# Performance work log

Hardware: AMD Instinct MI355X
Metric: run time of the kernel (lower is better)

Reference implementation:

```python
import jax, jax.numpy as jnp
import numpy as np

D_MODEL = 1024
N_HEADS = 16
HEAD_DIM = D_MODEL // N_HEADS
NEG_INF = -1e9


def setup_inputs() -> dict:
    key = jax.random.key(0)
    ks = jax.random.split(key, 6)
    B, T, C = 4, 2048, D_MODEL
    x = jax.random.normal(ks[0], (B, T, C), dtype=jnp.float32)
    # causal mask, broadcastable over batch and heads
    mask = jnp.tril(jnp.ones((T, T), dtype=jnp.int32))[None, None]
    scale = 1.0 / np.sqrt(C)
    W_qkv = jax.random.normal(ks[1], (3 * C, C), dtype=jnp.float32) * scale
    b_qkv = jnp.zeros((3 * C,), dtype=jnp.float32)
    W_out = jax.random.normal(ks[2], (C, C), dtype=jnp.float32) * scale
    b_out = jnp.zeros((C,), dtype=jnp.float32)
    return {"x": x, "mask": mask, "W_qkv": W_qkv, "b_qkv": b_qkv,
            "W_out": W_out, "b_out": b_out}


def reference(x, mask, W_qkv, b_qkv, W_out, b_out):
    B, T, C = x.shape
    H, D = N_HEADS, HEAD_DIM
    qkv = x @ W_qkv.T + b_qkv                      # [B, T, 3C]
    q, k, v = jnp.split(qkv, 3, axis=-1)
    # [B, T, C] -> [B, H, T, D]
    q = q.reshape(B, T, H, D).transpose(0, 2, 1, 3)
    k = k.reshape(B, T, H, D).transpose(0, 2, 1, 3)
    v = v.reshape(B, T, H, D).transpose(0, 2, 1, 3)
    scores = jnp.einsum("bhqd,bhkd->bhqk", q, k) / np.sqrt(D)
    scores = jnp.where(mask == 0, NEG_INF, scores)
    att = jax.nn.softmax(scores, axis=-1)          # dropout p=0 (eval)
    out = jnp.einsum("bhqk,bhkd->bhqd", att, v)    # [B, H, T, D]
    out = out.transpose(0, 2, 1, 3).reshape(B, T, C)
    return out @ W_out.T + b_out
```

## Files before the change

### kernel.cpp

```cpp
#include <hip/hip_runtime.h>
#include <hip/hip_bf16.h>

typedef unsigned short u16;
typedef unsigned int u32;
using short8 = __attribute__((ext_vector_type(8))) short;
using f32x4  = __attribute__((ext_vector_type(4))) float;
using f32x16 = __attribute__((ext_vector_type(16))) float;
using uint2v = __attribute__((ext_vector_type(2))) u32;

#define T_SEQ 2048
#define C_DIM 1024
#define NH 16
#define HD 64

#if __has_builtin(__builtin_amdgcn_exp2f)
#define EXP2(x) __builtin_amdgcn_exp2f(x)
#else
#define EXP2(x) exp2f(x)
#endif

__device__ __forceinline__ u16 f2bf(float f) {
    unsigned int u = __float_as_uint(f);
    unsigned int r = (u + 0x7fffu + ((u >> 16) & 1u)) >> 16;
    return (u16)r;
}
__device__ __forceinline__ u32 cvtpk(float lo, float hi) {
    u32 r;
    asm("v_cvt_pk_bf16_f32 %0, %1, %2" : "=v"(r) : "v"(lo), "v"(hi));
    return r;
}
__device__ __forceinline__ short8 mk8(u32 a, u32 b, u32 c, u32 d) {
    union { u32 u[4]; short8 s; } t;
    t.u[0] = a; t.u[1] = b; t.u[2] = c; t.u[3] = d;
    return t.s;
}
__device__ __forceinline__ void gl_lds16(const u16* g, u16* l) {
    __builtin_amdgcn_global_load_lds(
        (const __attribute__((address_space(1))) unsigned int*)g,
        (__attribute__((address_space(3))) unsigned int*)l, 16, 0, 0);
}
template <int N> __device__ __forceinline__ void s_vmcnt();
template <> __device__ __forceinline__ void s_vmcnt<0>() {
    asm volatile("s_waitcnt vmcnt(0)" ::: "memory");
}
template <> __device__ __forceinline__ void s_vmcnt<4>() {
    asm volatile("s_waitcnt vmcnt(4)" ::: "memory");
}
__device__ __forceinline__ void BAR() {
    asm volatile("" ::: "memory");
    __builtin_amdgcn_s_barrier();
    asm volatile("" ::: "memory");
}

__global__ __launch_bounds__(256) void cvt_f32_bf16(const float* __restrict__ in,
                                                    u16* __restrict__ out, int n8) {
    int i = blockIdx.x * blockDim.x + threadIdx.x;
    if (i >= n8) return;
    const float4* p = (const float4*)in + (size_t)i * 2;
    float4 a = p[0], b = p[1];
    short8 o;
    o[0] = (short)f2bf(a.x); o[1] = (short)f2bf(a.y);
    o[2] = (short)f2bf(a.z); o[3] = (short)f2bf(a.w);
    o[4] = (short)f2bf(b.x); o[5] = (short)f2bf(b.y);
    o[6] = (short)f2bf(b.z); o[7] = (short)f2bf(b.w);
    *(short8*)(out + (size_t)i * 8) = o;
}

template <int EPI>
__global__ __launch_bounds__(256) void gemm_bt(const u16* __restrict__ A,
                                               const u16* __restrict__ Bt,
                                               const float* __restrict__ bias,
                                               u16* __restrict__ qb, u16* __restrict__ kb,
                                               u16* __restrict__ vb, float* __restrict__ Cf,
                                               int M, int N, int K) {
    __shared__ __align__(16) u16 Al[2][128][32];
    __shared__ __align__(16) u16 Bl[2][128][32];
    const int tid = threadIdx.x;
    const int lane = tid & 63, wid = tid >> 6;
    const int li = lane & 15, g = lane >> 4;
    const int wr = (wid >> 1) * 64, wc = (wid & 1) * 64;
    const size_t m0 = (size_t)blockIdx.y * 128, n0 = (size_t)blockIdx.x * 128;

    const int srow = lane >> 2;
    const int sch = (lane & 3) ^ ((srow >> 1) & 3);
    const u16* aA = A + (m0 + wid * 32 + srow) * (size_t)K + sch * 8;
    const u16* aB = Bt + (n0 + wid * 32 + srow) * (size_t)K + sch * 8;

    f32x4 acc[4][4] = {};
    const int nt = K / 32;

    auto STAGE = [&](int buf, int k0) {
        gl_lds16(aA + k0, &Al[buf][wid * 32][0]);
        gl_lds16(aA + 16 * (size_t)K + k0, &Al[buf][wid * 32 + 16][0]);
        gl_lds16(aB + k0, &Bl[buf][wid * 32][0]);
        gl_lds16(aB + 16 * (size_t)K + k0, &Bl[buf][wid * 32 + 16][0]);
    };

    STAGE(0, 0);
#pragma unroll 2
    for (int t = 0; t < nt; ++t) {
        if (t + 1 < nt) { STAGE((t + 1) & 1, (t + 1) * 32); s_vmcnt<4>(); }
        else            { s_vmcnt<0>(); }
        BAR();
        short8 af[4], bf[4];
#pragma unroll
        for (int i = 0; i < 4; i++) {
            int row = wr + i * 16 + li;
            af[i] = *(const short8*)&Al[t & 1][row][(g ^ ((row >> 1) & 3)) * 8];
        }
#pragma unroll
        for (int i = 0; i < 4; i++) {
            int row = wc + i * 16 + li;
            bf[i] = *(const short8*)&Bl[t & 1][row][(g ^ ((row >> 1) & 3)) * 8];
        }
        __builtin_amdgcn_s_setprio(1);
#pragma unroll
        for (int mi = 0; mi < 4; mi++)
#pragma unroll
            for (int ni = 0; ni < 4; ni++)
                acc[mi][ni] = __builtin_amdgcn_mfma_f32_16x16x32_bf16(af[mi], bf[ni],
                                                                      acc[mi][ni], 0, 0, 0);
        __builtin_amdgcn_s_setprio(0);
        BAR();
    }

#pragma unroll
    for (int mi = 0; mi < 4; mi++)
#pragma unroll
        for (int ni = 0; ni < 4; ni++)
#pragma unroll
            for (int r = 0; r < 4; r++) {
                size_t row = m0 + wr + mi * 16 + g * 4 + r;
                size_t col = n0 + wc + ni * 16 + li;
                float val = acc[mi][ni][r] + bias[col];
                if (EPI == 0) {
                    int which = (int)(col >> 10);
                    int rem = (int)(col & 1023);
                    int h = rem >> 6, d = rem & 63;
                    size_t b = row >> 11, t = row & 2047;
                    if (which == 0) val *= 0.18033688f;
                    u16* dst = (which == 0) ? qb : (which == 1) ? kb : vb;
                    dst[(((b * NH) + h) * T_SEQ + t) * HD + d] = f2bf(val);
                } else {
                    Cf[row * (size_t)N + col] = val;
                }
            }
}

__global__ __launch_bounds__(256) void vtrans(const u16* __restrict__ V,
                                              u16* __restrict__ Vt) {
    __shared__ u16 L[128][72];
    const int tid = threadIdx.x;
    const int bh = blockIdx.y;
    const int t0 = blockIdx.x * 128;
    {
        int r = tid >> 1, cb = (tid & 1) * 32;
        const u16* src = V + ((size_t)bh * T_SEQ + t0 + r) * HD + cb;
#pragma unroll
        for (int j = 0; j < 4; j++)
            *(short8*)&L[r][cb + j * 8] = *(const short8*)(src + j * 8);
    }
    __syncthreads();
    {
        int d = tid >> 2, ts = (tid & 3) * 32;
        u16* dst = Vt + ((size_t)bh * HD + d) * T_SEQ + t0 + ts;
#pragma unroll
        for (int c = 0; c < 4; c++) {
            short8 o;
#pragma unroll
            for (int j = 0; j < 8; j++) o[j] = (short)L[ts + c * 8 + j][d];
            *(short8*)(dst + c * 8) = o;
        }
    }
}

__global__ __launch_bounds__(256) void attn_fwd2(const u16* __restrict__ Q,
                                                 const u16* __restrict__ K,
                                                 const u16* __restrict__ Vt,
                                                 u16* __restrict__ O) {
    __shared__ __align__(16) u16 KL[2][64 * 64];
    __shared__ __align__(16) u16 VL[2][64 * 64];
    const int tid = threadIdx.x;
    const int lane = tid & 63, wid = tid >> 6;
    const int l31 = lane & 31, hi = lane >> 5;

    const int wg = blockIdx.x;
    const int xcd = wg & 7, idx = wg >> 3;
    const int bh = (xcd << 3) | (idx >> 3);
    const int pair = idx & 7;
    const size_t bhT = (size_t)bh * T_SEQ;
    const int srow8 = lane >> 3, sch = lane & 7;
    const int b = bh >> 4, h = bh & 15;
    const int x7 = l31 & 7;

    for (int seg = 0; seg < 2; ++seg) {
        const int qt = seg ? pair : (15 - pair);
        const int q0 = qt * 128;
        const int qw0 = q0 + wid * 32;
        const int nkt = 2 * qt + 2;

        short8 qf[4];
        {
            const u16* qp = Q + (bhT + qw0 + l31) * HD + hi * 8;
#pragma unroll
            for (int s = 0; s < 4; s++) qf[s] = *(const short8*)(qp + s * 16);
        }

        f32x16 o0 = {}, o1 = {};
        float l_run = 0.f;

#pragma unroll
        for (int i = 0; i < 2; i++) {
            int row = wid * 16 + i * 8 + srow8;
            int ch = sch ^ (row & 7);
            gl_lds16(K + (bhT + row) * HD + ch * 8, &KL[0][(wid * 16 + i * 8) * 64]);
            gl_lds16(Vt + ((size_t)bh * HD + row) * T_SEQ + ch * 8,
                     &VL[0][(wid * 16 + i * 8) * 64]);
        }

        for (int kt = 0; kt < nkt; kt++) {
            __syncthreads();
            if (kt + 1 < nkt) {
                const int kv0n = (kt + 1) * 64;
                const int nb = (kt + 1) & 1;
#pragma unroll
                for (int i = 0; i < 2; i++) {
                    int row = wid * 16 + i * 8 + srow8;
                    int ch = sch ^ (row & 7);
                    gl_lds16(K + (bhT + kv0n + row) * HD + ch * 8,
                             &KL[nb][(wid * 16 + i * 8) * 64]);
                    gl_lds16(Vt + ((size_t)bh * HD + row) * T_SEQ + kv0n + ch * 8,
                             &VL[nb][(wid * 16 + i * 8) * 64]);
                }
            }
            const int kv0 = kt * 64;
            if (kv0 > qw0) continue;
            const u16* KLb = KL[kt & 1];
            const u16* VLb = VL[kt & 1];

            f32x16 s0 = {}, s1 = {};
            __builtin_amdgcn_s_setprio(1);
#pragma unroll
            for (int sl = 0; sl < 4; sl++) {
                int ch = ((sl * 2 + hi) ^ x7) * 8;
                short8 ka = *(const short8*)&KLb[l31 * 64 + ch];
                s0 = __builtin_amdgcn_mfma_f32_32x32x16_bf16(ka, qf[sl], s0, 0, 0, 0);
                short8 kb2 = *(const short8*)&KLb[(32 + l31) * 64 + ch];
                s1 = __builtin_amdgcn_mfma_f32_32x32x16_bf16(kb2, qf[sl], s1, 0, 0, 0);
            }
            __builtin_amdgcn_s_setprio(0);

            const int qg = qw0 + l31;
            if (kv0 + 63 > qw0) {
#pragma unroll
                for (int r = 0; r < 16; r++) {
                    int kvr = kv0 + (r & 3) + 8 * (r >> 2) + 4 * hi;
                    if (kvr > qg) s0[r] = -1e30f;
                    if (kvr + 32 > qg) s1[r] = -1e30f;
                }
            }

            float ls = 0.f;
#pragma unroll
            for (int r = 0; r < 16; r++) {
                float p0 = EXP2(s0[r]);
                float p1 = EXP2(s1[r]);
                s0[r] = p0; s1[r] = p1;
                ls += p0 + p1;
            }
            ls += __shfl_xor(ls, 32);
            l_run += ls;

            {
                u32 c0 = cvtpk(s0[0], s0[1]),   c1 = cvtpk(s0[2], s0[3]),
                    c2 = cvtpk(s0[4], s0[5]),   c3 = cvtpk(s0[6], s0[7]),
                    c4 = cvtpk(s0[8], s0[9]),   c5 = cvtpk(s0[10], s0[11]),
                    c6 = cvtpk(s0[12], s0[13]), c7 = cvtpk(s0[14], s0[15]);
                uint2v wA = __builtin_amdgcn_permlane32_swap(c0, c2, false, false);
                uint2v wB = __builtin_amdgcn_permlane32_swap(c1, c3, false, false);
                uint2v wC = __builtin_amdgcn_permlane32_swap(c4, c6, false, false);
                uint2v wD = __builtin_amdgcn_permlane32_swap(c5, c7, false, false);
                short8 paA = mk8(wA[0], wB[0], wA[1], wB[1]);
                short8 paB = mk8(wC[0], wD[0], wC[1], wD[1]);
                __builtin_amdgcn_s_setprio(1);
#pragma unroll
                for (int sl = 0; sl < 2; sl++) {
                    short8 pa = (sl == 0) ? paA : paB;
                    int ch = ((sl * 2 + hi) ^ x7) * 8;
                    short8 va = *(const short8*)&VLb[l31 * 64 + ch];
                    o0 = __builtin_amdgcn_mfma_f32_32x32x16_bf16(pa, va, o0, 0, 0, 0);
                    short8 vb2 = *(const short8*)&VLb[(32 + l31) * 64 + ch];
                    o1 = __builtin_amdgcn_mfma_f32_32x32x16_bf16(pa, vb2, o1, 0, 0, 0);
                }
                __builtin_amdgcn_s_setprio(0);
            }
            {
                u32 c0 = cvtpk(s1[0], s1[1]),   c1 = cvtpk(s1[2], s1[3]),
                    c2 = cvtpk(s1[4], s1[5]),   c3 = cvtpk(s1[6], s1[7]),
                    c4 = cvtpk(s1[8], s1[9]),   c5 = cvtpk(s1[10], s1[11]),
                    c6 = cvtpk(s1[12], s1[13]), c7 = cvtpk(s1[14], s1[15]);
                uint2v wA = __builtin_amdgcn_permlane32_swap(c0, c2, false, false);
                uint2v wB = __builtin_amdgcn_permlane32_swap(c1, c3, false, false);
                uint2v wC = __builtin_amdgcn_permlane32_swap(c4, c6, false, false);
                uint2v wD = __builtin_amdgcn_permlane32_swap(c5, c7, false, false);
                short8 paC = mk8(wA[0], wB[0], wA[1], wB[1]);
                short8 paD = mk8(wC[0], wD[0], wC[1], wD[1]);
                __builtin_amdgcn_s_setprio(1);
#pragma unroll
                for (int sl = 2; sl < 4; sl++) {
                    short8 pa = (sl == 2) ? paC : paD;
                    int ch = ((sl * 2 + hi) ^ x7) * 8;
                    short8 va = *(const short8*)&VLb[l31 * 64 + ch];
                    o0 = __builtin_amdgcn_mfma_f32_32x32x16_bf16(pa, va, o0, 0, 0, 0);
                    short8 vb2 = *(const short8*)&VLb[(32 + l31) * 64 + ch];
                    o1 = __builtin_amdgcn_mfma_f32_32x32x16_bf16(pa, vb2, o1, 0, 0, 0);
                }
                __builtin_amdgcn_s_setprio(0);
            }
        }

        const float inv = 1.0f / l_run;
#pragma unroll
        for (int r = 0; r < 16; r++) {
            int qr = (r & 3) + 8 * (r >> 2) + 4 * hi;
            float invr = __shfl(inv, qr);
            int t = q0 + wid * 32 + qr;
            size_t rowoff = ((size_t)b * T_SEQ + t) * C_DIM + h * HD;
            O[rowoff + l31]      = f2bf(o0[r] * invr);
            O[rowoff + 32 + l31] = f2bf(o1[r] * invr);
        }
    }
}

extern "C" void kernel_launch(void* const* d_in, const int* in_sizes, int n_in,
                              void* d_out, int out_size, void* d_ws, size_t ws_size,
                              hipStream_t stream) {
    const float* x     = (const float*)d_in[0];
    const float* W_qkv = (const float*)d_in[2];
    const float* b_qkv = (const float*)d_in[3];
    const float* W_out = (const float*)d_in[4];
    const float* b_out = (const float*)d_in[5];
    float* out = (float*)d_out;

    char* w = (char*)d_ws;
    u16* xb    = (u16*)(w);
    u16* wqkvb = (u16*)(w + 16777216);
    u16* woutb = (u16*)(w + 23068672);
    u16* qb    = (u16*)(w + 25165824);
    u16* kb    = (u16*)(w + 41943040);
    u16* vb    = (u16*)(w + 58720256);
    u16* vtb   = xb;
    u16* attnb = vb;

    cvt_f32_bf16<<<4096, 256, 0, stream>>>(x, xb, 1048576);
    cvt_f32_bf16<<<1536, 256, 0, stream>>>(W_qkv, wqkvb, 393216);
    cvt_f32_bf16<<<512, 256, 0, stream>>>(W_out, woutb, 131072);

    gemm_bt<0><<<dim3(24, 64), 256, 0, stream>>>(xb, wqkvb, b_qkv, qb, kb, vb, nullptr,
                                                 8192, 3072, 1024);

    vtrans<<<dim3(16, 64), 256, 0, stream>>>(vb, vtb);

    attn_fwd2<<<512, 256, 0, stream>>>(qb, kb, vtb, attnb);

    gemm_bt<1><<<dim3(8, 64), 256, 0, stream>>>(attnb, woutb, b_out, nullptr, nullptr,
                                                nullptr, out, 8192, 1024, 1024);
}
```

Before: 179.0 us.

## Fuse V transpose into QKV GEMM epilogue and split attention into per-tile blocks

The QKV GEMM epilogue now writes V directly in transposed [bh][d][t] layout with 4-wide vector stores, which removes the separate vtrans kernel and its extra round trip through memory. The attention kernel no longer loops over two paired q-tiles per block. It launches one block per q-tile (1024 blocks) and uses a new index mapping that interleaves heavy and light causal tiles. This gives finer scheduling granularity in exchange for dropping the explicit workload pairing. Q and K stores in the epilogue are restructured to hoist the bias load, and the workspace aliases are reassigned.

```diff
diff --git a/kernel.cpp b/kernel.cpp
--- a/kernel.cpp
+++ b/kernel.cpp
@@ -71,7 +71,7 @@
                                                const u16* __restrict__ Bt,
                                                const float* __restrict__ bias,
                                                u16* __restrict__ qb, u16* __restrict__ kb,
-                                               u16* __restrict__ vb, float* __restrict__ Cf,
+                                               u16* __restrict__ vtb, float* __restrict__ Cf,
                                                int M, int N, int K) {
     __shared__ __align__(16) u16 Al[2][128][32];
     __shared__ __align__(16) u16 Bl[2][128][32];
@@ -127,51 +127,37 @@
 #pragma unroll
     for (int mi = 0; mi < 4; mi++)
 #pragma unroll
-        for (int ni = 0; ni < 4; ni++)
-#pragma unroll
-            for (int r = 0; r < 4; r++) {
-                size_t row = m0 + wr + mi * 16 + g * 4 + r;
-                size_t col = n0 + wc + ni * 16 + li;
-                float val = acc[mi][ni][r] + bias[col];
-                if (EPI == 0) {
-                    int which = (int)(col >> 10);
-                    int rem = (int)(col & 1023);
-                    int h = rem >> 6, d = rem & 63;
-                    size_t b = row >> 11, t = row & 2047;
-                    if (which == 0) val *= 0.18033688f;
-                    u16* dst = (which == 0) ? qb : (which == 1) ? kb : vb;
-                    dst[(((b * NH) + h) * T_SEQ + t) * HD + d] = f2bf(val);
+        for (int ni = 0; ni < 4; ni++) {
+            size_t col = n0 + wc + ni * 16 + li;
+            size_t row0 = m0 + wr + mi * 16 + g * 4;
+            if (EPI == 0) {
+                int which = (int)(col >> 10);
+                int rem = (int)(col & 1023);
+                int h = rem >> 6, d = rem & 63;
+                size_t b = row0 >> 11, t0v = row0 & 2047;
+                float bv = bias[col];
+                if (which == 2) {
+                    ushort4 o4;
+                    o4.x = f2bf(acc[mi][ni][0] + bv);
+                    o4.y = f2bf(acc[mi][ni][1] + bv);
+                    o4.z = f2bf(acc[mi][ni][2] + bv);
+                    o4.w = f2bf(acc[mi][ni][3] + bv);
+                    *(ushort4*)(vtb + (((b * NH) + h) * (size_t)HD + d) * T_SEQ + t0v) = o4;
                 } else {
-                    Cf[row * (size_t)N + col] = val;
+                    u16* dst = (which == 0) ? qb : kb;
+                    float sc = (which == 0) ? 0.18033688f : 1.0f;
+#pragma unroll
+                    for (int r = 0; r < 4; r++)
+                        dst[(((b * NH) + h) * T_SEQ + t0v + r) * HD + d] =
+                            f2bf((acc[mi][ni][r] + bv) * sc);
                 }
-            }
-}
-
-__global__ __launch_bounds__(256) void vtrans(const u16* __restrict__ V,
-                                              u16* __restrict__ Vt) {
-    __shared__ u16 L[128][72];
-    const int tid = threadIdx.x;
-    const int bh = blockIdx.y;
-    const int t0 = blockIdx.x * 128;
-    {
-        int r = tid >> 1, cb = (tid & 1) * 32;
-        const u16* src = V + ((size_t)bh * T_SEQ + t0 + r) * HD + cb;
-#pragma unroll
-        for (int j = 0; j < 4; j++)
-            *(short8*)&L[r][cb + j * 8] = *(const short8*)(src + j * 8);
-    }
-    __syncthreads();
-    {
-        int d = tid >> 2, ts = (tid & 3) * 32;
-        u16* dst = Vt + ((size_t)bh * HD + d) * T_SEQ + t0 + ts;
-#pragma unroll
-        for (int c = 0; c < 4; c++) {
-            short8 o;
-#pragma unroll
-            for (int j = 0; j < 8; j++) o[j] = (short)L[ts + c * 8 + j][d];
-            *(short8*)(dst + c * 8) = o;
-        }
-    }
+            } else {
+                float bv = bias[col];
+#pragma unroll
+                for (int r = 0; r < 4; r++)
+                    Cf[(row0 + r) * (size_t)N + col] = acc[mi][ni][r] + bv;
+            }
+        }
 }
 
 __global__ __launch_bounds__(256) void attn_fwd2(const u16* __restrict__ Q,
@@ -184,151 +170,151 @@
     const int lane = tid & 63, wid = tid >> 6;
     const int l31 = lane & 31, hi = lane >> 5;
 
-    const int wg = blockIdx.x;
-    const int xcd = wg & 7, idx = wg >> 3;
-    const int bh = (xcd << 3) | (idx >> 3);
-    const int pair = idx & 7;
+    const int k = blockIdx.x;
+    const int j = k >> 8, c = k & 255;
+    const int u = c >> 4, v = c & 15;
+    const int bh = u * 4 + j;
+    const int a8 = (v + ((j >> 1) << 3)) & 15;
+    const int qt = (j & 1) ? (15 - a8) : a8;
+
     const size_t bhT = (size_t)bh * T_SEQ;
     const int srow8 = lane >> 3, sch = lane & 7;
     const int b = bh >> 4, h = bh & 15;
     const int x7 = l31 & 7;
 
-    for (int seg = 0; seg < 2; ++seg) {
-        const int qt = seg ? pair : (15 - pair);
-        const int q0 = qt * 128;
-        const int qw0 = q0 + wid * 32;
-        const int nkt = 2 * qt + 2;
-
-        short8 qf[4];
+    const int q0 = qt * 128;
+    const int qw0 = q0 + wid * 32;
+    const int nkt = 2 * qt + 2;
+
+    short8 qf[4];
+    {
+        const u16* qp = Q + (bhT + qw0 + l31) * HD + hi * 8;
+#pragma unroll
+        for (int s = 0; s < 4; s++) qf[s] = *(const short8*)(qp + s * 16);
+    }
+
+    f32x16 o0 = {}, o1 = {};
+    float l_run = 0.f;
+
+#pragma unroll
+    for (int i = 0; i < 2; i++) {
+        int row = wid * 16 + i * 8 + srow8;
+        int ch = sch ^ (row & 7);
+        gl_lds16(K + (bhT + row) * HD + ch * 8, &KL[0][(wid * 16 + i * 8) * 64]);
+        gl_lds16(Vt + ((size_t)bh * HD + row) * T_SEQ + ch * 8,
+                 &VL[0][(wid * 16 + i * 8) * 64]);
+    }
+
+    for (int kt = 0; kt < nkt; kt++) {
+        __syncthreads();
+        if (kt + 1 < nkt) {
+            const int kv0n = (kt + 1) * 64;
+            const int nb = (kt + 1) & 1;
+#pragma unroll
+            for (int i = 0; i < 2; i++) {
+                int row = wid * 16 + i * 8 + srow8;
+                int ch = sch ^ (row & 7);
+                gl_lds16(K + (bhT + kv0n + row) * HD + ch * 8,
+                         &KL[nb][(wid * 16 + i * 8) * 64]);
+                gl_lds16(Vt + ((size_t)bh * HD + row) * T_SEQ + kv0n + ch * 8,
+                         &VL[nb][(wid * 16 + i * 8) * 64]);
+            }
+        }
+        const int kv0 = kt * 64;
+        if (kv0 > qw0) continue;
+        const u16* KLb = KL[kt & 1];
+        const u16* VLb = VL[kt & 1];
+
+        f32x16 s0 = {}, s1 = {};
+        __builtin_amdgcn_s_setprio(1);
+#pragma unroll
+        for (int sl = 0; sl < 4; sl++) {
+            int ch = ((sl * 2 + hi) ^ x7) * 8;
+            short8 ka = *(const short8*)&KLb[l31 * 64 + ch];
+            s0 = __builtin_amdgcn_mfma_f32_32x32x16_bf16(ka, qf[sl], s0, 0, 0, 0);
+            short8 kb2 = *(const short8*)&KLb[(32 + l31) * 64 + ch];
+            s1 = __builtin_amdgcn_mfma_f32_32x32x16_bf16(kb2, qf[sl], s1, 0, 0, 0);
+        }
+        __builtin_amdgcn_s_setprio(0);
+
+        const int qg = qw0 + l31;
+        if (kv0 + 63 > qw0) {
+#pragma unroll
+            for (int r = 0; r < 16; r++) {
+                int kvr = kv0 + (r & 3) + 8 * (r >> 2) + 4 * hi;
+                if (kvr > qg) s0[r] = -1e30f;
+                if (kvr + 32 > qg) s1[r] = -1e30f;
+            }
+        }
+
+        float ls = 0.f;
+#pragma unroll
+        for (int r = 0; r < 16; r++) {
+            float p0 = EXP2(s0[r]);
+            float p1 = EXP2(s1[r]);
+            s0[r] = p0; s1[r] = p1;
+            ls += p0 + p1;
+        }
+        ls += __shfl_xor(ls, 32);
+        l_run += ls;
+
         {
-            const u16* qp = Q + (bhT + qw0 + l31) * HD + hi * 8;
-#pragma unroll
-            for (int s = 0; s < 4; s++) qf[s] = *(const short8*)(qp + s * 16);
-        }
-
-        f32x16 o0 = {}, o1 = {};
-        float l_run = 0.f;
-
-#pragma unroll
-        for (int i = 0; i < 2; i++) {
-            int row = wid * 16 + i * 8 + srow8;
-            int ch = sch ^ (row & 7);
-            gl_lds16(K + (bhT + row) * HD + ch * 8, &KL[0][(wid * 16 + i * 8) * 64]);
-            gl_lds16(Vt + ((size_t)bh * HD + row) * T_SEQ + ch * 8,
-                     &VL[0][(wid * 16 + i * 8) * 64]);
-        }
-
-        for (int kt = 0; kt < nkt; kt++) {
-            __syncthreads();
-            if (kt + 1 < nkt) {
-                const int kv0n = (kt + 1) * 64;
-                const int nb = (kt + 1) & 1;
-#pragma unroll
-                for (int i = 0; i < 2; i++) {
-                    int row = wid * 16 + i * 8 + srow8;
-                    int ch = sch ^ (row & 7);
-                    gl_lds16(K + (bhT + kv0n + row) * HD + ch * 8,
-                             &KL[nb][(wid * 16 + i * 8) * 64]);
-                    gl_lds16(Vt + ((size_t)bh * HD + row) * T_SEQ + kv0n + ch * 8,
-                             &VL[nb][(wid * 16 + i * 8) * 64]);
-                }
-            }
-            const int kv0 = kt * 64;
-            if (kv0 > qw0) continue;
-            const u16* KLb = KL[kt & 1];
-            const u16* VLb = VL[kt & 1];
-
-            f32x16 s0 = {}, s1 = {};
+            u32 c0 = cvtpk(s0[0], s0[1]),   c1 = cvtpk(s0[2], s0[3]),
+                c2 = cvtpk(s0[4], s0[5]),   c3 = cvtpk(s0[6], s0[7]),
+                c4 = cvtpk(s0[8], s0[9]),   c5 = cvtpk(s0[10], s0[11]),
+                c6 = cvtpk(s0[12], s0[13]), c7 = cvtpk(s0[14], s0[15]);
+            uint2v wA = __builtin_amdgcn_permlane32_swap(c0, c2, false, false);
+            uint2v wB = __builtin_amdgcn_permlane32_swap(c1, c3, false, false);
+            uint2v wC = __builtin_amdgcn_permlane32_swap(c4, c6, false, false);
+            uint2v wD = __builtin_amdgcn_permlane32_swap(c5, c7, false, false);
+            short8 paA = mk8(wA[0], wB[0], wA[1], wB[1]);
+            short8 paB = mk8(wC[0], wD[0], wC[1], wD[1]);
             __builtin_amdgcn_s_setprio(1);
 #pragma unroll
-            for (int sl = 0; sl < 4; sl++) {
+            for (int sl = 0; sl < 2; sl++) {
+                short8 pa = (sl == 0) ? paA : paB;
                 int ch = ((sl * 2 + hi) ^ x7) * 8;
-                short8 ka = *(const short8*)&KLb[l31 * 64 + ch];
-                s0 = __builtin_amdgcn_mfma_f32_32x32x16_bf16(ka, qf[sl], s0, 0, 0, 0);
-                short8 kb2 = *(const short8*)&KLb[(32 + l31) * 64 + ch];
-                s1 = __builtin_amdgcn_mfma_f32_32x32x16_bf16(kb2, qf[sl], s1, 0, 0, 0);
+                short8 va = *(const short8*)&VLb[l31 * 64 + ch];
+                o0 = __builtin_amdgcn_mfma_f32_32x32x16_bf16(pa, va, o0, 0, 0, 0);
+                short8 vb2 = *(const short8*)&VLb[(32 + l31) * 64 + ch];
+                o1 = __builtin_amdgcn_mfma_f32_32x32x16_bf16(pa, vb2, o1, 0, 0, 0);
             }
             __builtin_amdgcn_s_setprio(0);
-
-            const int qg = qw0 + l31;
-            if (kv0 + 63 > qw0) {
-#pragma unroll
-                for (int r = 0; r < 16; r++) {
-                    int kvr = kv0 + (r & 3) + 8 * (r >> 2) + 4 * hi;
-                    if (kvr > qg) s0[r] = -1e30f;
-                    if (kvr + 32 > qg) s1[r] = -1e30f;
-                }
-            }
-
-            float ls = 0.f;
-#pragma unroll
-            for (int r = 0; r < 16; r++) {
-                float p0 = EXP2(s0[r]);
-                float p1 = EXP2(s1[r]);
-                s0[r] = p0; s1[r] = p1;
-                ls += p0 + p1;
-            }
-            ls += __shfl_xor(ls, 32);
-            l_run += ls;
-
-            {
-                u32 c0 = cvtpk(s0[0], s0[1]),   c1 = cvtpk(s0[2], s0[3]),
-                    c2 = cvtpk(s0[4], s0[5]),   c3 = cvtpk(s0[6], s0[7]),
-                    c4 = cvtpk(s0[8], s0[9]),   c5 = cvtpk(s0[10], s0[11]),
-                    c6 = cvtpk(s0[12], s0[13]), c7 = cvtpk(s0[14], s0[15]);
-                uint2v wA = __builtin_amdgcn_permlane32_swap(c0, c2, false, false);
-                uint2v wB = __builtin_amdgcn_permlane32_swap(c1, c3, false, false);
-                uint2v wC = __builtin_amdgcn_permlane32_swap(c4, c6, false, false);
-                uint2v wD = __builtin_amdgcn_permlane32_swap(c5, c7, false, false);
-                short8 paA = mk8(wA[0], wB[0], wA[1], wB[1]);
-                short8 paB = mk8(wC[0], wD[0], wC[1], wD[1]);
-                __builtin_amdgcn_s_setprio(1);
-#pragma unroll
-                for (int sl = 0; sl < 2; sl++) {
-                    short8 pa = (sl == 0) ? paA : paB;
-                    int ch = ((sl * 2 + hi) ^ x7) * 8;
-                    short8 va = *(const short8*)&VLb[l31 * 64 + ch];
-                    o0 = __builtin_amdgcn_mfma_f32_32x32x16_bf16(pa, va, o0, 0, 0, 0);
-                    short8 vb2 = *(const short8*)&VLb[(32 + l31) * 64 + ch];
-                    o1 = __builtin_amdgcn_mfma_f32_32x32x16_bf16(pa, vb2, o1, 0, 0, 0);
-                }
-                __builtin_amdgcn_s_setprio(0);
-            }
-            {
-                u32 c0 = cvtpk(s1[0], s1[1]),   c1 = cvtpk(s1[2], s1[3]),
-                    c2 = cvtpk(s1[4], s1[5]),   c3 = cvtpk(s1[6], s1[7]),
-                    c4 = cvtpk(s1[8], s1[9]),   c5 = cvtpk(s1[10], s1[11]),
-                    c6 = cvtpk(s1[12], s1[13]), c7 = cvtpk(s1[14], s1[15]);
-                uint2v wA = __builtin_amdgcn_permlane32_swap(c0, c2, false, false);
-                uint2v wB = __builtin_amdgcn_permlane32_swap(c1, c3, false, false);
-                uint2v wC = __builtin_amdgcn_permlane32_swap(c4, c6, false, false);
-                uint2v wD = __builtin_amdgcn_permlane32_swap(c5, c7, false, false);
-                short8 paC = mk8(wA[0], wB[0], wA[1], wB[1]);
-                short8 paD = mk8(wC[0], wD[0], wC[1], wD[1]);
-                __builtin_amdgcn_s_setprio(1);
-#pragma unroll
-                for (int sl = 2; sl < 4; sl++) {
-                    short8 pa = (sl == 2) ? paC : paD;
-                    int ch = ((sl * 2 + hi) ^ x7) * 8;
-                    short8 va = *(const short8*)&VLb[l31 * 64 + ch];
-                    o0 = __builtin_amdgcn_mfma_f32_32x32x16_bf16(pa, va, o0, 0, 0, 0);
-                    short8 vb2 = *(const short8*)&VLb[(32 + l31) * 64 + ch];
-                    o1 = __builtin_amdgcn_mfma_f32_32x32x16_bf16(pa, vb2, o1, 0, 0, 0);
-                }
-                __builtin_amdgcn_s_setprio(0);
-            }
-        }
-
-        const float inv = 1.0f / l_run;
-#pragma unroll
-        for (int r = 0; r < 16; r++) {
-            int qr = (r & 3) + 8 * (r >> 2) + 4 * hi;
-            float invr = __shfl(inv, qr);
-            int t = q0 + wid * 32 + qr;
-            size_t rowoff = ((size_t)b * T_SEQ + t) * C_DIM + h * HD;
-            O[rowoff + l31]      = f2bf(o0[r] * invr);
-            O[rowoff + 32 + l31] = f2bf(o1[r] * invr);
-        }
+        }
+        {
+            u32 c0 = cvtpk(s1[0], s1[1]),   c1 = cvtpk(s1[2], s1[3]),
+                c2 = cvtpk(s1[4], s1[5]),   c3 = cvtpk(s1[6], s1[7]),
+                c4 = cvtpk(s1[8], s1[9]),   c5 = cvtpk(s1[10], s1[11]),
+                c6 = cvtpk(s1[12], s1[13]), c7 = cvtpk(s1[14], s1[15]);
+            uint2v wA = __builtin_amdgcn_permlane32_swap(c0, c2, false, false);
+            uint2v wB = __builtin_amdgcn_permlane32_swap(c1, c3, false, false);
+            uint2v wC = __builtin_amdgcn_permlane32_swap(c4, c6, false, false);
+            uint2v wD = __builtin_amdgcn_permlane32_swap(c5, c7, false, false);
+            short8 paC = mk8(wA[0], wB[0], wA[1], wB[1]);
+            short8 paD = mk8(wC[0], wD[0], wC[1], wD[1]);
+            __builtin_amdgcn_s_setprio(1);
+#pragma unroll
+            for (int sl = 2; sl < 4; sl++) {
+                short8 pa = (sl == 2) ? paC : paD;
+                int ch = ((sl * 2 + hi) ^ x7) * 8;
+                short8 va = *(const short8*)&VLb[l31 * 64 + ch];
+                o0 = __builtin_amdgcn_mfma_f32_32x32x16_bf16(pa, va, o0, 0, 0, 0);
+                short8 vb2 = *(const short8*)&VLb[(32 + l31) * 64 + ch];
+                o1 = __builtin_amdgcn_mfma_f32_32x32x16_bf16(pa, vb2, o1, 0, 0, 0);
+            }
+            __builtin_amdgcn_s_setprio(0);
+        }
+    }
+
+    const float inv = 1.0f / l_run;
+#pragma unroll
+    for (int r = 0; r < 16; r++) {
+        int qr = (r & 3) + 8 * (r >> 2) + 4 * hi;
+        float invr = __shfl(inv, qr);
+        int t = q0 + wid * 32 + qr;
+        size_t rowoff = ((size_t)b * T_SEQ + t) * C_DIM + h * HD;
+        O[rowoff + l31]      = f2bf(o0[r] * invr);
+        O[rowoff + 32 + l31] = f2bf(o1[r] * invr);
     }
 }
 
@@ -348,20 +334,17 @@
     u16* woutb = (u16*)(w + 23068672);
     u16* qb    = (u16*)(w + 25165824);
     u16* kb    = (u16*)(w + 41943040);
-    u16* vb    = (u16*)(w + 58720256);
-    u16* vtb   = xb;
-    u16* attnb = vb;
+    u16* vtb   = (u16*)(w + 58720256);
+    u16* attnb = xb;
 
     cvt_f32_bf16<<<4096, 256, 0, stream>>>(x, xb, 1048576);
     cvt_f32_bf16<<<1536, 256, 0, stream>>>(W_qkv, wqkvb, 393216);
     cvt_f32_bf16<<<512, 256, 0, stream>>>(W_out, woutb, 131072);
 
-    gemm_bt<0><<<dim3(24, 64), 256, 0, stream>>>(xb, wqkvb, b_qkv, qb, kb, vb, nullptr,
+    gemm_bt<0><<<dim3(24, 64), 256, 0, stream>>>(xb, wqkvb, b_qkv, qb, kb, vtb, nullptr,
                                                  8192, 3072, 1024);
 
-    vtrans<<<dim3(16, 64), 256, 0, stream>>>(vb, vtb);
-
-    attn_fwd2<<<512, 256, 0, stream>>>(qb, kb, vtb, attnb);
+    attn_fwd2<<<1024, 256, 0, stream>>>(qb, kb, vtb, attnb);
 
     gemm_bt<1><<<dim3(8, 64), 256, 0, stream>>>(attnb, woutb, b_out, nullptr, nullptr,
                                                 nullptr, out, 8192, 1024, 1024);
```

Result: no change. 181.5 us (median of 2 runs) (+1.4%).
